# Performance work log

Hardware: AMD Instinct MI355X
Metric: run time of the kernel (lower is better)

The kernel has to match this reference:

```python
import jax, jax.numpy as jnp
import numpy as np

B, T, N, D = 16, 12, 512, 128
H, DH = 4, 32            # heads, per-head dim (out_dim = H*DH = 128)
E = 4096                  # edges in the static road graph
NEG_SLOPE = 0.2
LN_EPS = 1e-5


def setup_inputs() -> dict:
    key = jax.random.key(0)
    ks = jax.random.split(key, 9)
    x = jax.random.normal(ks[0], (B, T, N, D), dtype=jnp.float32)
    edge_index = jax.random.randint(ks[1], (2, E), 0, N, dtype=jnp.int64)
    edge_weight = jax.random.uniform(ks[2], (E,), dtype=jnp.float32)
    # GAT parameters (dropout in eval mode -> identity)
    W = jax.random.normal(ks[3], (D, H * DH), dtype=jnp.float32) * (1.0 / np.sqrt(D))
    att_src = jax.random.normal(ks[4], (H, DH), dtype=jnp.float32) * 0.1
    att_dst = jax.random.normal(ks[5], (H, DH), dtype=jnp.float32) * 0.1
    bias = jnp.zeros((H * DH,), dtype=jnp.float32)
    ln_gamma = jnp.ones((H * DH,), dtype=jnp.float32)
    ln_beta = jnp.zeros((H * DH,), dtype=jnp.float32)
    return {"x": x, "edge_index": edge_index, "edge_weight": edge_weight,
            "W": W, "att_src": att_src, "att_dst": att_dst, "bias": bias,
            "ln_gamma": ln_gamma, "ln_beta": ln_beta}


def reference(x, edge_index, edge_weight, W, att_src, att_dst, bias, ln_gamma, ln_beta):
    b, t, n, din = x.shape
    bt = b * t
    h_heads, dh = att_src.shape
    src, dst = edge_index[0], edge_index[1]

    # project: [BT, N, H, DH]
    h = (x.reshape(bt, n, din) @ W).reshape(bt, n, h_heads, dh)

    # per-node attention scores, then gather to edges: [BT, E, H]
    s_src = jnp.einsum('bnhd,hd->bnh', h, att_src)
    s_dst = jnp.einsum('bnhd,hd->bnh', h, att_dst)
    e = jax.nn.leaky_relu(s_src[:, src] + s_dst[:, dst], NEG_SLOPE)
    e = e * edge_weight[None, :, None]  # edge_weight modulates attention logits

    # scatter-softmax over incoming edges per destination node
    m = jnp.full((bt, n, h_heads), -1e30, dtype=e.dtype).at[:, dst].max(e)
    ex = jnp.exp(e - m[:, dst])
    denom = jnp.zeros((bt, n, h_heads), dtype=e.dtype).at[:, dst].add(ex)
    alpha = ex / (denom[:, dst] + 1e-16)  # [BT, E, H]

    # weighted aggregation (scatter-add) of source features
    msg = alpha[..., None] * h[:, src]  # [BT, E, H, DH]
    agg = jnp.zeros((bt, n, h_heads, dh), dtype=h.dtype).at[:, dst].add(msg)

    out = agg.reshape(b, t, n, h_heads * dh) + bias

    # LayerNorm then ELU
    mu = out.mean(axis=-1, keepdims=True)
    var = out.var(axis=-1, keepdims=True)
    out = (out - mu) * jax.lax.rsqrt(var + LN_EPS) * ln_gamma + ln_beta
    return jnp.where(out > 0, out, jnp.expm1(out))
```

## Files before the change

### kernel.cpp

```cpp
#include <hip/hip_runtime.h>

#define BT    192
#define NNODE 512
#define DIM   128
#define NH    4
#define DH    32
#define NE    4096
#define NROWS (BT * NNODE)

typedef __attribute__((ext_vector_type(8))) short  short8b;
typedef __attribute__((ext_vector_type(4))) float  floatx4;
typedef __attribute__((ext_vector_type(8))) unsigned short ushort8;

__device__ inline unsigned short f2bf(float f) {
    unsigned int u = __float_as_uint(f);
    return (unsigned short)((u + 0x7FFFu + ((u >> 16) & 1u)) >> 16);
}
__device__ inline float bflo(unsigned int v) { return __uint_as_float(v << 16); }
__device__ inline float bfhi(unsigned int v) { return __uint_as_float(v & 0xFFFF0000u); }

__device__ inline short8b pack8(float4 a, float4 b) {
    short8b r;
    r[0] = (short)f2bf(a.x); r[1] = (short)f2bf(a.y);
    r[2] = (short)f2bf(a.z); r[3] = (short)f2bf(a.w);
    r[4] = (short)f2bf(b.x); r[5] = (short)f2bf(b.y);
    r[6] = (short)f2bf(b.z); r[7] = (short)f2bf(b.w);
    return r;
}

__global__ __launch_bounds__(512) void csr_build_k(
    const int* __restrict__ ei, const float* __restrict__ ew,
    const float* __restrict__ W,
    int* __restrict__ row_ptr2, int* __restrict__ csr_src,
    float* __restrict__ csr_ew, int* __restrict__ perm,
    unsigned short* __restrict__ wswz)
{
    __shared__ int dsts[NE];
    __shared__ int cnt[NNODE];
    __shared__ int scan[NNODE];
    __shared__ int nodeAt[NNODE];
    __shared__ int hist[256];
    __shared__ int hscan[256];
    int t = threadIdx.x;
    int b = blockIdx.x;

    if (b >= 64) {
        int j = (b - 64) * 512 + t;
        const float4* W4 = (const float4*)W;
        float4 wv = W4[j];
        int k = j >> 5, c4 = (j & 31) * 4;
        float vv[4] = { wv.x, wv.y, wv.z, wv.w };
#pragma unroll
        for (int e = 0; e < 4; ++e) {
            int col = c4 + e;
            int byte = col * 256 + ((2 * k) ^ ((col & 7) << 4));
            wswz[byte >> 1] = f2bf(vv[e]);
        }
        return;
    }

    for (int e = t; e < NE; e += 512) dsts[e] = ei[NE + e];
    cnt[t] = 0;
    if (t < 256) hist[t] = 0;
    __syncthreads();
    for (int e = t; e < NE; e += 512) atomicAdd(&cnt[dsts[e]], 1);
    __syncthreads();

    int deg = cnt[t];
    int bkt = (deg < 255) ? deg : 255;
    atomicAdd(&hist[bkt], 1);
    __syncthreads();
    if (t < 256) hscan[t] = hist[t];
    __syncthreads();
    for (int o = 1; o < 256; o <<= 1) {
        int v = (t < 256 && t >= o) ? hscan[t - o] : 0;
        __syncthreads();
        if (t < 256) hscan[t] += v;
        __syncthreads();
    }
    int off = 0;
    for (int n = 0; n < t; ++n) {
        int dn = cnt[n]; dn = (dn < 255) ? dn : 255;
        off += (dn == bkt) ? 1 : 0;
    }
    int rank = hscan[bkt] - hist[bkt] + off;
    nodeAt[rank] = t;
    __syncthreads();

    scan[t] = cnt[nodeAt[t]];
    __syncthreads();
    for (int o = 1; o < NNODE; o <<= 1) {
        int v = (t >= o) ? scan[t - o] : 0;
        __syncthreads();
        scan[t] += v;
        __syncthreads();
    }
    if (b == 0) {
        if (t == 0) row_ptr2[0] = 0;
        row_ptr2[t + 1] = scan[t];
        perm[t] = nodeAt[t];
    }
    __syncthreads();

    int wave = t >> 6, lane = t & 63;
    int r = b * 8 + wave;
    int node = nodeAt[r];
    int pos = scan[r] - cnt[node];
    for (int c = 0; c < NE; c += 64) {
        int e = c + lane;
        int d = dsts[e];
        unsigned long long mask = __ballot(d == node);
        if (d == node) {
            int ofs = __popcll(mask & ((1ull << lane) - 1ull));
            csr_src[pos + ofs] = ei[e];
            csr_ew[pos + ofs]  = ew[e];
        }
        pos += __popcll(mask);
    }
}

__global__ __launch_bounds__(256) void gemm_mfma_k(
    const float* __restrict__ x, const unsigned short* __restrict__ wswz,
    const float* __restrict__ att_src, const float* __restrict__ att_dst,
    unsigned short* __restrict__ h, float* __restrict__ ssg,
    float* __restrict__ sdg)
{
    __shared__ __align__(16) char sm[64 * 132 * 4];
    __shared__ float att_f[256];
    int t = threadIdx.x;
    if (t < 128) att_f[t] = att_src[(t & 3) * 32 + (t >> 2)];
    else         att_f[t] = att_dst[(t & 3) * 32 + ((t - 128) >> 2)];
    {
        const uint4* g = (const uint4*)wswz;
        uint4* ld = (uint4*)sm;
#pragma unroll
        for (int i = 0; i < 8; ++i) ld[t + i * 256] = g[t + i * 256];
    }
    int w = t >> 6, l = t & 63, lr = l & 15, lk = l >> 4;
    size_t base = (size_t)blockIdx.x * 128;
    const float* xA = x + (base + (size_t)w * 16 + lr) * DIM;
    const float* xB = xA + 64 * DIM;

    floatx4 accA[8], accB[8];
#pragma unroll
    for (int n = 0; n < 8; ++n) {
        accA[n] = (floatx4){0.f, 0.f, 0.f, 0.f};
        accB[n] = (floatx4){0.f, 0.f, 0.f, 0.f};
    }
    __syncthreads();

#pragma unroll
    for (int kk = 0; kk < 4; ++kk) {
        int k0 = kk * 32 + lk * 8;
        float4 a0 = *(const float4*)(xA + k0);
        float4 a1 = *(const float4*)(xA + k0 + 4);
        float4 b0 = *(const float4*)(xB + k0);
        float4 b1 = *(const float4*)(xB + k0 + 4);
        short8b av = pack8(a0, a1);
        short8b bv = pack8(b0, b1);
        int c = kk * 4 + lk;
#pragma unroll
        for (int n = 0; n < 8; ++n) {
            int col = n * 16 + lr;
            short8b bf = *(const short8b*)(sm + col * 256 + ((c ^ (col & 7)) << 4));
            accA[n] = __builtin_amdgcn_mfma_f32_16x16x32_bf16(av, bf, accA[n], 0, 0, 0);
            accB[n] = __builtin_amdgcn_mfma_f32_16x16x32_bf16(bv, bf, accB[n], 0, 0, 0);
        }
    }

    float* Ct = (float*)sm;
    unsigned short* hbase = h + base * DIM;
    int sr = t >> 2, sq = t & 3;

    __syncthreads();
#pragma unroll
    for (int n = 0; n < 8; ++n)
#pragma unroll
        for (int j = 0; j < 4; ++j)
            Ct[(w * 16 + lk * 4 + j) * 132 + n * 16 + lr] = accA[n][j];
    __syncthreads();
#pragma unroll
    for (int i = 0; i < 4; ++i) {
        int chunk = t + i * 256;
        int row = chunk >> 4, cc = chunk & 15;
        const float* cp = Ct + row * 132 + cc * 8;
        ushort8 v;
#pragma unroll
        for (int e = 0; e < 8; ++e) v[e] = f2bf(cp[e]);
        *(ushort8*)(hbase + row * DIM + cc * 8) = v;
    }
    {
        const float* cp = Ct + sr * 132 + sq * 32;
        float ps = 0.f, pd = 0.f;
#pragma unroll
        for (int j = 0; j < 32; j += 4) {
            float4 cv = *(const float4*)(cp + j);
            ps = fmaf(cv.x, att_f[(j+0)*4 + sq], ps);
            ps = fmaf(cv.y, att_f[(j+1)*4 + sq], ps);
            ps = fmaf(cv.z, att_f[(j+2)*4 + sq], ps);
            ps = fmaf(cv.w, att_f[(j+3)*4 + sq], ps);
            pd = fmaf(cv.x, att_f[128 + (j+0)*4 + sq], pd);
            pd = fmaf(cv.y, att_f[128 + (j+1)*4 + sq], pd);
            pd = fmaf(cv.z, att_f[128 + (j+2)*4 + sq], pd);
            pd = fmaf(cv.w, att_f[128 + (j+3)*4 + sq], pd);
        }
        size_t grow = base + sr;
        ssg[grow * 4 + sq] = ps;
        sdg[grow * 4 + sq] = pd;
    }

    __syncthreads();
#pragma unroll
    for (int n = 0; n < 8; ++n)
#pragma unroll
        for (int j = 0; j < 4; ++j)
            Ct[(w * 16 + lk * 4 + j) * 132 + n * 16 + lr] = accB[n][j];
    __syncthreads();
#pragma unroll
    for (int i = 0; i < 4; ++i) {
        int chunk = t + i * 256;
        int row = chunk >> 4, cc = chunk & 15;
        const float* cp = Ct + row * 132 + cc * 8;
        ushort8 v;
#pragma unroll
        for (int e = 0; e < 8; ++e) v[e] = f2bf(cp[e]);
        *(ushort8*)(hbase + (64 + row) * DIM + cc * 8) = v;
    }
    {
        const float* cp = Ct + sr * 132 + sq * 32;
        float ps = 0.f, pd = 0.f;
#pragma unroll
        for (int j = 0; j < 32; j += 4) {
            float4 cv = *(const float4*)(cp + j);
            ps = fmaf(cv.x, att_f[(j+0)*4 + sq], ps);
            ps = fmaf(cv.y, att_f[(j+1)*4 + sq], ps);
            ps = fmaf(cv.z, att_f[(j+2)*4 + sq], ps);
            ps = fmaf(cv.w, att_f[(j+3)*4 + sq], ps);
            pd = fmaf(cv.x, att_f[128 + (j+0)*4 + sq], pd);
            pd = fmaf(cv.y, att_f[128 + (j+1)*4 + sq], pd);
            pd = fmaf(cv.z, att_f[128 + (j+2)*4 + sq], pd);
            pd = fmaf(cv.w, att_f[128 + (j+3)*4 + sq], pd);
        }
        size_t grow = base + 64 + sr;
        ssg[grow * 4 + sq] = ps;
        sdg[grow * 4 + sq] = pd;
    }
}

__global__ __launch_bounds__(1024) void agg_ln_k(
    const unsigned short* __restrict__ h,
    const float* __restrict__ ssg, const float* __restrict__ sdg,
    const int* __restrict__ rp2, const int* __restrict__ cs2,
    const float* __restrict__ ce2, const int* __restrict__ perm,
    const float* __restrict__ bias, const float* __restrict__ gamma,
    const float* __restrict__ beta, float* __restrict__ out)
{
    __shared__ unsigned int hs[NH][NNODE * 16];
    __shared__ float ssl[NNODE * NH];
    __shared__ float prm[384];
    int t  = threadIdx.x;
    int bt = blockIdx.x;

    const uint4* hg = (const uint4*)(h + (size_t)bt * NNODE * DIM);
    for (int i = t; i < NNODE * 16; i += 1024) {
        int n = i >> 4, c = i & 15, hh = c >> 2, j = c & 3;
        uint4 v = hg[i];
        int js = j ^ ((n >> 1) & 3);
        *(uint4*)&hs[hh][n * 16 + js * 4] = v;
    }
    const float* ssgb = ssg + (size_t)bt * NNODE * NH;
    for (int i = t; i < NNODE * NH; i += 1024) ssl[i] = ssgb[i];
    if (t < 384) prm[t] = (t < 128) ? bias[t] : (t < 256) ? gamma[t - 128] : beta[t - 256];
    __syncthreads();

    int l  = t & 63, w = t >> 6;
    int hh = l >> 4, rl = l & 15;
    int g  = w * 16 + rl;
    const float* sdgb = sdg + (size_t)bt * NNODE * NH;
    float* outb = out + (size_t)bt * NNODE * DIM;

#pragma unroll
    for (int pi = 0; pi < 2; ++pi) {
        int rank = pi ? (511 - g) : g;
        int node = perm[rank];
        int beg = rp2[rank], end = rp2[rank + 1];
        float sd = sdgb[node * 4 + hh];

        float acc[32];
#pragma unroll
        for (int d = 0; d < 32; ++d) acc[d] = 0.f;
        float den = 0.f;

        for (int e = beg; e < end; ++e) {
            int   s  = cs2[e];
            float wt = ce2[e];
            float a = ssl[s * 4 + hh] + sd;
            a = (a > 0.f) ? a : 0.2f * a;
            float p = __expf(a * wt);
            den += p;
            const unsigned int* hr = &hs[hh][s * 16];
            int sx = (s >> 1) & 3;
#pragma unroll
            for (int j = 0; j < 4; ++j) {
                uint4 v = *(const uint4*)&hr[(j ^ sx) * 4];
                int d0 = j * 8;
                acc[d0+0] = fmaf(p, bflo(v.x), acc[d0+0]);
                acc[d0+1] = fmaf(p, bfhi(v.x), acc[d0+1]);
                acc[d0+2] = fmaf(p, bflo(v.y), acc[d0+2]);
                acc[d0+3] = fmaf(p, bfhi(v.y), acc[d0+3]);
                acc[d0+4] = fmaf(p, bflo(v.z), acc[d0+4]);
                acc[d0+5] = fmaf(p, bfhi(v.z), acc[d0+5]);
                acc[d0+6] = fmaf(p, bflo(v.w), acc[d0+6]);
                acc[d0+7] = fmaf(p, bfhi(v.w), acc[d0+7]);
            }
        }

        float inv = 1.f / (den + 1e-16f);
        float s1 = 0.f, s2 = 0.f;
#pragma unroll
        for (int d = 0; d < 32; ++d) {
            float vv = fmaf(acc[d], inv, prm[hh * 32 + d]);
            acc[d] = vv;
            s1 += vv;
            s2 = fmaf(vv, vv, s2);
        }
        s1 += __shfl_xor(s1, 16, 64);
        s2 += __shfl_xor(s2, 16, 64);
        s1 += __shfl_xor(s1, 32, 64);
        s2 += __shfl_xor(s2, 32, 64);
        float mean = s1 * (1.f / 128.f);
        float var  = s2 * (1.f / 128.f) - mean * mean;
        float rstd = rsqrtf(var + 1e-5f);

        float* op = outb + (size_t)node * DIM + hh * 32;
#pragma unroll
        for (int d = 0; d < 32; d += 4) {
            int pd0 = 128 + hh * 32 + d, pb0 = 256 + hh * 32 + d;
            float y0 = (acc[d+0] - mean) * rstd * prm[pd0+0] + prm[pb0+0];
            float y1 = (acc[d+1] - mean) * rstd * prm[pd0+1] + prm[pb0+1];
            float y2 = (acc[d+2] - mean) * rstd * prm[pd0+2] + prm[pb0+2];
            float y3 = (acc[d+3] - mean) * rstd * prm[pd0+3] + prm[pb0+3];
            float4 o4;
            o4.x = (y0 > 0.f) ? y0 : expm1f(y0);
            o4.y = (y1 > 0.f) ? y1 : expm1f(y1);
            o4.z = (y2 > 0.f) ? y2 : expm1f(y2);
            o4.w = (y3 > 0.f) ? y3 : expm1f(y3);
            *(float4*)(op + d) = o4;
        }
    }
}

extern "C" void kernel_launch(void* const* d_in, const int* in_sizes, int n_in,
                              void* d_out, int out_size, void* d_ws, size_t ws_size,
                              hipStream_t stream)
{
    const float* x     = (const float*)d_in[0];
    const int*   ei    = (const int*)  d_in[1];
    const float* ew    = (const float*)d_in[2];
    const float* W     = (const float*)d_in[3];
    const float* asrc  = (const float*)d_in[4];
    const float* adst  = (const float*)d_in[5];
    const float* bias  = (const float*)d_in[6];
    const float* gamma = (const float*)d_in[7];
    const float* beta  = (const float*)d_in[8];
    float* out = (float*)d_out;

    char* ws = (char*)d_ws;
    unsigned short* h = (unsigned short*)ws;
    size_t off = (size_t)NROWS * DIM * sizeof(unsigned short);
    unsigned short* wswz = (unsigned short*)(ws + off);
    off += (size_t)DIM * DIM * sizeof(unsigned short);
    float* ssg = (float*)(ws + off);
    off += (size_t)NROWS * NH * sizeof(float);
    float* sdg = (float*)(ws + off);
    off += (size_t)NROWS * NH * sizeof(float);
    int* rp2 = (int*)(ws + off);
    off += (((NNODE + 1) * sizeof(int)) + 15) & ~(size_t)15;
    int* perm = (int*)(ws + off);
    off += (size_t)NNODE * sizeof(int);
    int* cs2 = (int*)(ws + off);
    off += (size_t)NE * sizeof(int);
    float* ce2 = (float*)(ws + off);
    off += (size_t)NE * sizeof(float);

    csr_build_k<<<72, 512, 0, stream>>>(ei, ew, W, rp2, cs2, ce2, perm, wswz);
    gemm_mfma_k<<<NROWS / 128, 256, 0, stream>>>(x, wswz, asrc, adst, h, ssg, sdg);
    agg_ln_k<<<BT, 1024, 0, stream>>>(h, ssg, sdg, rp2, cs2, ce2, perm,
                                      bias, gamma, beta, out);
}
```

Before: 73.24 us.

## Stage LayerNorm output through shared memory for coalesced row stores

The shared h buffer becomes one flat array laid out in two head-pair halves with an 8-way XOR swizzle, and it is reused after aggregation as a staging area for the output. Each thread keeps both passes' results in registers (64 floats), writes them to shared memory, then the block reads them back so that whole 512-byte node rows go out as contiguous float4 stores. The goal is better-coalesced global writes in place of per-thread 128-byte strided stores. In exchange the kernel needs more registers, extra barriers and extra shared-memory traffic.

```diff
diff --git a/kernel.cpp b/kernel.cpp
--- a/kernel.cpp
+++ b/kernel.cpp
@@ -255,18 +255,19 @@
     const float* __restrict__ bias, const float* __restrict__ gamma,
     const float* __restrict__ beta, float* __restrict__ out)
 {
-    __shared__ unsigned int hs[NH][NNODE * 16];
+    __shared__ __align__(16) unsigned int smem[NNODE * 64];
     __shared__ float ssl[NNODE * NH];
     __shared__ float prm[384];
     int t  = threadIdx.x;
     int bt = blockIdx.x;
 
     const uint4* hg = (const uint4*)(h + (size_t)bt * NNODE * DIM);
+    uint4* hs4 = (uint4*)smem;
     for (int i = t; i < NNODE * 16; i += 1024) {
-        int n = i >> 4, c = i & 15, hh = c >> 2, j = c & 3;
+        int n = i >> 4, c = i & 15;
         uint4 v = hg[i];
-        int js = j ^ ((n >> 1) & 3);
-        *(uint4*)&hs[hh][n * 16 + js * 4] = v;
+        int cp = (c & 7) ^ (n & 7);
+        hs4[(c >> 3) * 4096 + n * 8 + cp] = v;
     }
     const float* ssgb = ssg + (size_t)bt * NNODE * NH;
     for (int i = t; i < NNODE * NH; i += 1024) ssl[i] = ssgb[i];
@@ -276,8 +277,11 @@
     int l  = t & 63, w = t >> 6;
     int hh = l >> 4, rl = l & 15;
     int g  = w * 16 + rl;
+    int pair = hh >> 1, sub = hh & 1;
     const float* sdgb = sdg + (size_t)bt * NNODE * NH;
     float* outb = out + (size_t)bt * NNODE * DIM;
+
+    float y[2][32];
 
 #pragma unroll
     for (int pi = 0; pi < 2; ++pi) {
@@ -285,11 +289,9 @@
         int node = perm[rank];
         int beg = rp2[rank], end = rp2[rank + 1];
         float sd = sdgb[node * 4 + hh];
-
-        float acc[32];
-#pragma unroll
-        for (int d = 0; d < 32; ++d) acc[d] = 0.f;
         float den = 0.f;
+#pragma unroll
+        for (int d = 0; d < 32; ++d) y[pi][d] = 0.f;
 
         for (int e = beg; e < end; ++e) {
             int   s  = cs2[e];
@@ -298,20 +300,20 @@
             a = (a > 0.f) ? a : 0.2f * a;
             float p = __expf(a * wt);
             den += p;
-            const unsigned int* hr = &hs[hh][s * 16];
-            int sx = (s >> 1) & 3;
+            const uint4* hr = hs4 + pair * 4096 + s * 8;
+            int sx = s & 7;
 #pragma unroll
             for (int j = 0; j < 4; ++j) {
-                uint4 v = *(const uint4*)&hr[(j ^ sx) * 4];
+                uint4 v = hr[(sub * 4 + j) ^ sx];
                 int d0 = j * 8;
-                acc[d0+0] = fmaf(p, bflo(v.x), acc[d0+0]);
-                acc[d0+1] = fmaf(p, bfhi(v.x), acc[d0+1]);
-                acc[d0+2] = fmaf(p, bflo(v.y), acc[d0+2]);
-                acc[d0+3] = fmaf(p, bfhi(v.y), acc[d0+3]);
-                acc[d0+4] = fmaf(p, bflo(v.z), acc[d0+4]);
-                acc[d0+5] = fmaf(p, bfhi(v.z), acc[d0+5]);
-                acc[d0+6] = fmaf(p, bflo(v.w), acc[d0+6]);
-                acc[d0+7] = fmaf(p, bfhi(v.w), acc[d0+7]);
+                y[pi][d0+0] = fmaf(p, bflo(v.x), y[pi][d0+0]);
+                y[pi][d0+1] = fmaf(p, bfhi(v.x), y[pi][d0+1]);
+                y[pi][d0+2] = fmaf(p, bflo(v.y), y[pi][d0+2]);
+                y[pi][d0+3] = fmaf(p, bfhi(v.y), y[pi][d0+3]);
+                y[pi][d0+4] = fmaf(p, bflo(v.z), y[pi][d0+4]);
+                y[pi][d0+5] = fmaf(p, bfhi(v.z), y[pi][d0+5]);
+                y[pi][d0+6] = fmaf(p, bflo(v.w), y[pi][d0+6]);
+                y[pi][d0+7] = fmaf(p, bfhi(v.w), y[pi][d0+7]);
             }
         }
 
@@ -319,8 +321,8 @@
         float s1 = 0.f, s2 = 0.f;
 #pragma unroll
         for (int d = 0; d < 32; ++d) {
-            float vv = fmaf(acc[d], inv, prm[hh * 32 + d]);
-            acc[d] = vv;
+            float vv = fmaf(y[pi][d], inv, prm[hh * 32 + d]);
+            y[pi][d] = vv;
             s1 += vv;
             s2 = fmaf(vv, vv, s2);
         }
@@ -331,21 +333,33 @@
         float mean = s1 * (1.f / 128.f);
         float var  = s2 * (1.f / 128.f) - mean * mean;
         float rstd = rsqrtf(var + 1e-5f);
-
-        float* op = outb + (size_t)node * DIM + hh * 32;
-#pragma unroll
-        for (int d = 0; d < 32; d += 4) {
-            int pd0 = 128 + hh * 32 + d, pb0 = 256 + hh * 32 + d;
-            float y0 = (acc[d+0] - mean) * rstd * prm[pd0+0] + prm[pb0+0];
-            float y1 = (acc[d+1] - mean) * rstd * prm[pd0+1] + prm[pb0+1];
-            float y2 = (acc[d+2] - mean) * rstd * prm[pd0+2] + prm[pb0+2];
-            float y3 = (acc[d+3] - mean) * rstd * prm[pd0+3] + prm[pb0+3];
-            float4 o4;
-            o4.x = (y0 > 0.f) ? y0 : expm1f(y0);
-            o4.y = (y1 > 0.f) ? y1 : expm1f(y1);
-            o4.z = (y2 > 0.f) ? y2 : expm1f(y2);
-            o4.w = (y3 > 0.f) ? y3 : expm1f(y3);
-            *(float4*)(op + d) = o4;
+#pragma unroll
+        for (int d = 0; d < 32; ++d) {
+            float yy = (y[pi][d] - mean) * rstd * prm[128 + hh * 32 + d]
+                     + prm[256 + hh * 32 + d];
+            y[pi][d] = (yy > 0.f) ? yy : expm1f(yy);
+        }
+    }
+
+    float4* st = (float4*)smem;
+#pragma unroll
+    for (int pi = 0; pi < 2; ++pi) {
+        __syncthreads();
+#pragma unroll
+        for (int j = 0; j < 8; ++j) {
+            int m  = hh * 8 + j;
+            int mp = m ^ (g & 31);
+            float4 v = { y[pi][j*4+0], y[pi][j*4+1], y[pi][j*4+2], y[pi][j*4+3] };
+            st[g * 32 + mp] = v;
+        }
+        __syncthreads();
+#pragma unroll
+        for (int k = 0; k < 8; ++k) {
+            int c = t + k * 1024;
+            int r = c >> 5, m = c & 31;
+            float4 v = st[r * 32 + (m ^ (r & 31))];
+            int rank = pi ? (511 - r) : r;
+            *(float4*)(outb + (size_t)perm[rank] * DIM + m * 4) = v;
         }
     }
 }
```

Measured after the change: 77.90 us. 1.06x slower.

## Gather source rows from global memory instead of staging in LDS; split nodes across two blocks

Applied to the files above, without the earlier changes.

The aggregation kernel no longer copies each timestep's full h tile (128 KB of bf16) and source scores into shared memory. It gathers source rows directly from global memory, relying on cache. Work is split across twice as many blocks, each handling alternating degree ranks. The 4 heads of a node now sit in adjacent lanes, so the LayerNorm reduction uses shuffles at distances 1 and 2, and the edge loop is unrolled by two so more loads are in flight. This removes the LDS staging cost and the large LDS footprint that limited occupancy, at the cost of uncoalesced global gathers.

```diff
diff --git a/kernel.cpp b/kernel.cpp
--- a/kernel.cpp
+++ b/kernel.cpp
@@ -255,98 +255,113 @@
     const float* __restrict__ bias, const float* __restrict__ gamma,
     const float* __restrict__ beta, float* __restrict__ out)
 {
-    __shared__ unsigned int hs[NH][NNODE * 16];
-    __shared__ float ssl[NNODE * NH];
     __shared__ float prm[384];
-    int t  = threadIdx.x;
-    int bt = blockIdx.x;
-
-    const uint4* hg = (const uint4*)(h + (size_t)bt * NNODE * DIM);
-    for (int i = t; i < NNODE * 16; i += 1024) {
-        int n = i >> 4, c = i & 15, hh = c >> 2, j = c & 3;
-        uint4 v = hg[i];
-        int js = j ^ ((n >> 1) & 3);
-        *(uint4*)&hs[hh][n * 16 + js * 4] = v;
-    }
-    const float* ssgb = ssg + (size_t)bt * NNODE * NH;
-    for (int i = t; i < NNODE * NH; i += 1024) ssl[i] = ssgb[i];
+    int t = threadIdx.x;
     if (t < 384) prm[t] = (t < 128) ? bias[t] : (t < 256) ? gamma[t - 128] : beta[t - 256];
     __syncthreads();
 
-    int l  = t & 63, w = t >> 6;
-    int hh = l >> 4, rl = l & 15;
-    int g  = w * 16 + rl;
-    const float* sdgb = sdg + (size_t)bt * NNODE * NH;
-    float* outb = out + (size_t)bt * NNODE * DIM;
-
-#pragma unroll
-    for (int pi = 0; pi < 2; ++pi) {
-        int rank = pi ? (511 - g) : g;
-        int node = perm[rank];
-        int beg = rp2[rank], end = rp2[rank + 1];
-        float sd = sdgb[node * 4 + hh];
-
-        float acc[32];
-#pragma unroll
-        for (int d = 0; d < 32; ++d) acc[d] = 0.f;
-        float den = 0.f;
-
-        for (int e = beg; e < end; ++e) {
-            int   s  = cs2[e];
-            float wt = ce2[e];
-            float a = ssl[s * 4 + hh] + sd;
-            a = (a > 0.f) ? a : 0.2f * a;
-            float p = __expf(a * wt);
-            den += p;
-            const unsigned int* hr = &hs[hh][s * 16];
-            int sx = (s >> 1) & 3;
-#pragma unroll
-            for (int j = 0; j < 4; ++j) {
-                uint4 v = *(const uint4*)&hr[(j ^ sx) * 4];
-                int d0 = j * 8;
-                acc[d0+0] = fmaf(p, bflo(v.x), acc[d0+0]);
-                acc[d0+1] = fmaf(p, bfhi(v.x), acc[d0+1]);
-                acc[d0+2] = fmaf(p, bflo(v.y), acc[d0+2]);
-                acc[d0+3] = fmaf(p, bfhi(v.y), acc[d0+3]);
-                acc[d0+4] = fmaf(p, bflo(v.z), acc[d0+4]);
-                acc[d0+5] = fmaf(p, bfhi(v.z), acc[d0+5]);
-                acc[d0+6] = fmaf(p, bflo(v.w), acc[d0+6]);
-                acc[d0+7] = fmaf(p, bfhi(v.w), acc[d0+7]);
-            }
-        }
-
-        float inv = 1.f / (den + 1e-16f);
-        float s1 = 0.f, s2 = 0.f;
-#pragma unroll
-        for (int d = 0; d < 32; ++d) {
-            float vv = fmaf(acc[d], inv, prm[hh * 32 + d]);
-            acc[d] = vv;
-            s1 += vv;
-            s2 = fmaf(vv, vv, s2);
-        }
-        s1 += __shfl_xor(s1, 16, 64);
-        s2 += __shfl_xor(s2, 16, 64);
-        s1 += __shfl_xor(s1, 32, 64);
-        s2 += __shfl_xor(s2, 32, 64);
-        float mean = s1 * (1.f / 128.f);
-        float var  = s2 * (1.f / 128.f) - mean * mean;
-        float rstd = rsqrtf(var + 1e-5f);
-
-        float* op = outb + (size_t)node * DIM + hh * 32;
-#pragma unroll
-        for (int d = 0; d < 32; d += 4) {
-            int pd0 = 128 + hh * 32 + d, pb0 = 256 + hh * 32 + d;
-            float y0 = (acc[d+0] - mean) * rstd * prm[pd0+0] + prm[pb0+0];
-            float y1 = (acc[d+1] - mean) * rstd * prm[pd0+1] + prm[pb0+1];
-            float y2 = (acc[d+2] - mean) * rstd * prm[pd0+2] + prm[pb0+2];
-            float y3 = (acc[d+3] - mean) * rstd * prm[pd0+3] + prm[pb0+3];
-            float4 o4;
-            o4.x = (y0 > 0.f) ? y0 : expm1f(y0);
-            o4.y = (y1 > 0.f) ? y1 : expm1f(y1);
-            o4.z = (y2 > 0.f) ? y2 : expm1f(y2);
-            o4.w = (y3 > 0.f) ? y3 : expm1f(y3);
-            *(float4*)(op + d) = o4;
-        }
+    int bt   = blockIdx.x >> 1;
+    int par  = blockIdx.x & 1;
+    int hh   = t & 3;
+    int rank = ((t >> 2) << 1) + par;
+    int node = perm[rank];
+    int beg  = rp2[rank], end = rp2[rank + 1];
+
+    const unsigned short* hb = h + (size_t)bt * NNODE * DIM;
+    const float* ssb = ssg + (size_t)bt * NNODE * NH;
+    float sd = sdg[((size_t)bt * NNODE + node) * NH + hh];
+
+    float acc[32];
+#pragma unroll
+    for (int d = 0; d < 32; ++d) acc[d] = 0.f;
+    float den = 0.f;
+
+    int e = beg;
+    for (; e + 2 <= end; e += 2) {
+        int   s0 = cs2[e],   s1 = cs2[e + 1];
+        float w0 = ce2[e],   w1 = ce2[e + 1];
+        float a0 = ssb[s0 * 4 + hh] + sd; a0 = (a0 > 0.f) ? a0 : 0.2f * a0;
+        float a1 = ssb[s1 * 4 + hh] + sd; a1 = (a1 > 0.f) ? a1 : 0.2f * a1;
+        float p0 = __expf(a0 * w0);
+        float p1 = __expf(a1 * w1);
+        den += p0; den += p1;
+        const uint4* r0 = (const uint4*)(hb + (size_t)s0 * DIM) + hh * 4;
+        const uint4* r1 = (const uint4*)(hb + (size_t)s1 * DIM) + hh * 4;
+#pragma unroll
+        for (int j = 0; j < 4; ++j) {
+            uint4 v0 = r0[j];
+            uint4 v1 = r1[j];
+            int d0 = j * 8;
+            acc[d0+0] = fmaf(p0, bflo(v0.x), acc[d0+0]);
+            acc[d0+1] = fmaf(p0, bfhi(v0.x), acc[d0+1]);
+            acc[d0+2] = fmaf(p0, bflo(v0.y), acc[d0+2]);
+            acc[d0+3] = fmaf(p0, bfhi(v0.y), acc[d0+3]);
+            acc[d0+4] = fmaf(p0, bflo(v0.z), acc[d0+4]);
+            acc[d0+5] = fmaf(p0, bfhi(v0.z), acc[d0+5]);
+            acc[d0+6] = fmaf(p0, bflo(v0.w), acc[d0+6]);
+            acc[d0+7] = fmaf(p0, bfhi(v0.w), acc[d0+7]);
+            acc[d0+0] = fmaf(p1, bflo(v1.x), acc[d0+0]);
+            acc[d0+1] = fmaf(p1, bfhi(v1.x), acc[d0+1]);
+            acc[d0+2] = fmaf(p1, bflo(v1.y), acc[d0+2]);
+            acc[d0+3] = fmaf(p1, bfhi(v1.y), acc[d0+3]);
+            acc[d0+4] = fmaf(p1, bflo(v1.z), acc[d0+4]);
+            acc[d0+5] = fmaf(p1, bfhi(v1.z), acc[d0+5]);
+            acc[d0+6] = fmaf(p1, bflo(v1.w), acc[d0+6]);
+            acc[d0+7] = fmaf(p1, bfhi(v1.w), acc[d0+7]);
+        }
+    }
+    if (e < end) {
+        int   s0 = cs2[e];
+        float w0 = ce2[e];
+        float a0 = ssb[s0 * 4 + hh] + sd; a0 = (a0 > 0.f) ? a0 : 0.2f * a0;
+        float p0 = __expf(a0 * w0);
+        den += p0;
+        const uint4* r0 = (const uint4*)(hb + (size_t)s0 * DIM) + hh * 4;
+#pragma unroll
+        for (int j = 0; j < 4; ++j) {
+            uint4 v0 = r0[j];
+            int d0 = j * 8;
+            acc[d0+0] = fmaf(p0, bflo(v0.x), acc[d0+0]);
+            acc[d0+1] = fmaf(p0, bfhi(v0.x), acc[d0+1]);
+            acc[d0+2] = fmaf(p0, bflo(v0.y), acc[d0+2]);
+            acc[d0+3] = fmaf(p0, bfhi(v0.y), acc[d0+3]);
+            acc[d0+4] = fmaf(p0, bflo(v0.z), acc[d0+4]);
+            acc[d0+5] = fmaf(p0, bfhi(v0.z), acc[d0+5]);
+            acc[d0+6] = fmaf(p0, bflo(v0.w), acc[d0+6]);
+            acc[d0+7] = fmaf(p0, bfhi(v0.w), acc[d0+7]);
+        }
+    }
+
+    float inv = 1.f / (den + 1e-16f);
+    float s1 = 0.f, s2 = 0.f;
+#pragma unroll
+    for (int d = 0; d < 32; ++d) {
+        float vv = fmaf(acc[d], inv, prm[hh * 32 + d]);
+        acc[d] = vv;
+        s1 += vv;
+        s2 = fmaf(vv, vv, s2);
+    }
+    s1 += __shfl_xor(s1, 1, 64);
+    s2 += __shfl_xor(s2, 1, 64);
+    s1 += __shfl_xor(s1, 2, 64);
+    s2 += __shfl_xor(s2, 2, 64);
+    float mean = s1 * (1.f / 128.f);
+    float var  = s2 * (1.f / 128.f) - mean * mean;
+    float rstd = rsqrtf(var + 1e-5f);
+
+    float* op = out + ((size_t)bt * NNODE + node) * DIM + hh * 32;
+#pragma unroll
+    for (int d = 0; d < 32; d += 4) {
+        float y0 = (acc[d+0] - mean) * rstd * prm[128 + hh*32 + d+0] + prm[256 + hh*32 + d+0];
+        float y1 = (acc[d+1] - mean) * rstd * prm[128 + hh*32 + d+1] + prm[256 + hh*32 + d+1];
+        float y2 = (acc[d+2] - mean) * rstd * prm[128 + hh*32 + d+2] + prm[256 + hh*32 + d+2];
+        float y3 = (acc[d+3] - mean) * rstd * prm[128 + hh*32 + d+3] + prm[256 + hh*32 + d+3];
+        float4 o4;
+        o4.x = (y0 > 0.f) ? y0 : expm1f(y0);
+        o4.y = (y1 > 0.f) ? y1 : expm1f(y1);
+        o4.z = (y2 > 0.f) ? y2 : expm1f(y2);
+        o4.w = (y3 > 0.f) ? y3 : expm1f(y3);
+        *(float4*)(op + d) = o4;
     }
 }
 
@@ -385,6 +400,6 @@
 
     csr_build_k<<<72, 512, 0, stream>>>(ei, ew, W, rp2, cs2, ce2, perm, wswz);
     gemm_mfma_k<<<NROWS / 128, 256, 0, stream>>>(x, wswz, asrc, adst, h, ssg, sdg);
-    agg_ln_k<<<BT, 1024, 0, stream>>>(h, ssg, sdg, rp2, cs2, ce2, perm,
-                                      bias, gamma, beta, out);
-}
+    agg_ln_k<<<BT * 2, 1024, 0, stream>>>(h, ssg, sdg, rp2, cs2, ce2, perm,
+                                          bias, gamma, beta, out);
+}
```

Result: slower. 100.2 us (+36.8%).

## Fold CSR build into GEMM launch as extra blocks and unroll edge loop

Applied to the files above, without the earlier changes.

The CSR construction moves out of its own kernel and into 64 extra blocks of the GEMM launch. These blocks reuse the GEMM's shared memory and use 256 threads, each handling two nodes. A small kernel now only swizzles W to bf16, so the serial CSR build runs alongside the projection GEMM instead of before it. The aggregation edge loop is also unrolled by 4 so index loads and exps from several edges can overlap. In exchange the CSR blocks do twice the per-thread serial rank work, and the unrolled loop raises register pressure.

```diff
diff --git a/kernel.cpp b/kernel.cpp
--- a/kernel.cpp
+++ b/kernel.cpp
@@ -7,6 +7,7 @@
 #define DH    32
 #define NE    4096
 #define NROWS (BT * NNODE)
+#define GEMM_BLOCKS (NROWS / 128)
 
 typedef __attribute__((ext_vector_type(8))) short  short8b;
 typedef __attribute__((ext_vector_type(4))) float  floatx4;
@@ -28,94 +29,34 @@
     return r;
 }
 
-__global__ __launch_bounds__(512) void csr_build_k(
-    const int* __restrict__ ei, const float* __restrict__ ew,
-    const float* __restrict__ W,
-    int* __restrict__ row_ptr2, int* __restrict__ csr_src,
-    float* __restrict__ csr_ew, int* __restrict__ perm,
-    unsigned short* __restrict__ wswz)
+#define EDGE_ACC(hrow, sx, p) do {                                   \
+    _Pragma("unroll")                                                \
+    for (int j = 0; j < 4; ++j) {                                    \
+        uint4 v = *(const uint4*)&(hrow)[(j ^ (sx)) * 4];            \
+        int d0 = j * 8;                                              \
+        acc[d0+0] = fmaf((p), bflo(v.x), acc[d0+0]);                 \
+        acc[d0+1] = fmaf((p), bfhi(v.x), acc[d0+1]);                 \
+        acc[d0+2] = fmaf((p), bflo(v.y), acc[d0+2]);                 \
+        acc[d0+3] = fmaf((p), bfhi(v.y), acc[d0+3]);                 \
+        acc[d0+4] = fmaf((p), bflo(v.z), acc[d0+4]);                 \
+        acc[d0+5] = fmaf((p), bfhi(v.z), acc[d0+5]);                 \
+        acc[d0+6] = fmaf((p), bflo(v.w), acc[d0+6]);                 \
+        acc[d0+7] = fmaf((p), bfhi(v.w), acc[d0+7]);                 \
+    } } while (0)
+
+__global__ __launch_bounds__(512) void wswz_k(
+    const float* __restrict__ W, unsigned short* __restrict__ wswz)
 {
-    __shared__ int dsts[NE];
-    __shared__ int cnt[NNODE];
-    __shared__ int scan[NNODE];
-    __shared__ int nodeAt[NNODE];
-    __shared__ int hist[256];
-    __shared__ int hscan[256];
-    int t = threadIdx.x;
-    int b = blockIdx.x;
-
-    if (b >= 64) {
-        int j = (b - 64) * 512 + t;
-        const float4* W4 = (const float4*)W;
-        float4 wv = W4[j];
-        int k = j >> 5, c4 = (j & 31) * 4;
-        float vv[4] = { wv.x, wv.y, wv.z, wv.w };
-#pragma unroll
-        for (int e = 0; e < 4; ++e) {
-            int col = c4 + e;
-            int byte = col * 256 + ((2 * k) ^ ((col & 7) << 4));
-            wswz[byte >> 1] = f2bf(vv[e]);
-        }
-        return;
-    }
-
-    for (int e = t; e < NE; e += 512) dsts[e] = ei[NE + e];
-    cnt[t] = 0;
-    if (t < 256) hist[t] = 0;
-    __syncthreads();
-    for (int e = t; e < NE; e += 512) atomicAdd(&cnt[dsts[e]], 1);
-    __syncthreads();
-
-    int deg = cnt[t];
-    int bkt = (deg < 255) ? deg : 255;
-    atomicAdd(&hist[bkt], 1);
-    __syncthreads();
-    if (t < 256) hscan[t] = hist[t];
-    __syncthreads();
-    for (int o = 1; o < 256; o <<= 1) {
-        int v = (t < 256 && t >= o) ? hscan[t - o] : 0;
-        __syncthreads();
-        if (t < 256) hscan[t] += v;
-        __syncthreads();
-    }
-    int off = 0;
-    for (int n = 0; n < t; ++n) {
-        int dn = cnt[n]; dn = (dn < 255) ? dn : 255;
-        off += (dn == bkt) ? 1 : 0;
-    }
-    int rank = hscan[bkt] - hist[bkt] + off;
-    nodeAt[rank] = t;
-    __syncthreads();
-
-    scan[t] = cnt[nodeAt[t]];
-    __syncthreads();
-    for (int o = 1; o < NNODE; o <<= 1) {
-        int v = (t >= o) ? scan[t - o] : 0;
-        __syncthreads();
-        scan[t] += v;
-        __syncthreads();
-    }
-    if (b == 0) {
-        if (t == 0) row_ptr2[0] = 0;
-        row_ptr2[t + 1] = scan[t];
-        perm[t] = nodeAt[t];
-    }
-    __syncthreads();
-
-    int wave = t >> 6, lane = t & 63;
-    int r = b * 8 + wave;
-    int node = nodeAt[r];
-    int pos = scan[r] - cnt[node];
-    for (int c = 0; c < NE; c += 64) {
-        int e = c + lane;
-        int d = dsts[e];
-        unsigned long long mask = __ballot(d == node);
-        if (d == node) {
-            int ofs = __popcll(mask & ((1ull << lane) - 1ull));
-            csr_src[pos + ofs] = ei[e];
-            csr_ew[pos + ofs]  = ew[e];
-        }
-        pos += __popcll(mask);
+    int j = blockIdx.x * 512 + threadIdx.x;
+    const float4* W4 = (const float4*)W;
+    float4 wv = W4[j];
+    int k = j >> 5, c4 = (j & 31) * 4;
+    float vv[4] = { wv.x, wv.y, wv.z, wv.w };
+#pragma unroll
+    for (int e = 0; e < 4; ++e) {
+        int col = c4 + e;
+        int byte = col * 256 + ((2 * k) ^ ((col & 7) << 4));
+        wswz[byte >> 1] = f2bf(vv[e]);
     }
 }
 
@@ -123,11 +64,101 @@
     const float* __restrict__ x, const unsigned short* __restrict__ wswz,
     const float* __restrict__ att_src, const float* __restrict__ att_dst,
     unsigned short* __restrict__ h, float* __restrict__ ssg,
-    float* __restrict__ sdg)
+    float* __restrict__ sdg,
+    const int* __restrict__ ei, const float* __restrict__ ew,
+    int* __restrict__ rp2, int* __restrict__ cs2,
+    float* __restrict__ ce2, int* __restrict__ perm)
 {
     __shared__ __align__(16) char sm[64 * 132 * 4];
     __shared__ float att_f[256];
     int t = threadIdx.x;
+
+    if (blockIdx.x >= GEMM_BLOCKS) {
+        int* dsts   = (int*)sm;
+        int* cnt    = (int*)(sm + 16384);
+        int* scn    = (int*)(sm + 18432);
+        int* nodeAt = (int*)(sm + 20480);
+        int* hist   = (int*)(sm + 22528);
+        int* hscan  = (int*)(sm + 23552);
+        int cb = blockIdx.x - GEMM_BLOCKS;
+        int i0 = t, i1 = t + 256;
+
+        for (int e = t; e < NE; e += 256) dsts[e] = ei[NE + e];
+        cnt[i0] = 0; cnt[i1] = 0;
+        hist[t] = 0;
+        __syncthreads();
+        for (int e = t; e < NE; e += 256) atomicAdd(&cnt[dsts[e]], 1);
+        __syncthreads();
+
+        int deg0 = cnt[i0], deg1 = cnt[i1];
+        int b0 = (deg0 < 255) ? deg0 : 255;
+        int b1 = (deg1 < 255) ? deg1 : 255;
+        atomicAdd(&hist[b0], 1);
+        atomicAdd(&hist[b1], 1);
+        __syncthreads();
+        hscan[t] = hist[t];
+        __syncthreads();
+        for (int o = 1; o < 256; o <<= 1) {
+            int v = (t >= o) ? hscan[t - o] : 0;
+            __syncthreads();
+            hscan[t] += v;
+            __syncthreads();
+        }
+        int off0 = 0, off1 = 0;
+        for (int n = 0; n < i0; ++n) {
+            int dn = cnt[n]; dn = (dn < 255) ? dn : 255;
+            off0 += (dn == b0) ? 1 : 0;
+        }
+        for (int n = 0; n < i1; ++n) {
+            int dn = cnt[n]; dn = (dn < 255) ? dn : 255;
+            off1 += (dn == b1) ? 1 : 0;
+        }
+        int rank0 = hscan[b0] - hist[b0] + off0;
+        int rank1 = hscan[b1] - hist[b1] + off1;
+        nodeAt[rank0] = i0;
+        nodeAt[rank1] = i1;
+        __syncthreads();
+
+        scn[i0] = cnt[nodeAt[i0]];
+        scn[i1] = cnt[nodeAt[i1]];
+        __syncthreads();
+        for (int o = 1; o < NNODE; o <<= 1) {
+            int v0 = (i0 >= o) ? scn[i0 - o] : 0;
+            int v1 = (i1 >= o) ? scn[i1 - o] : 0;
+            __syncthreads();
+            scn[i0] += v0; scn[i1] += v1;
+            __syncthreads();
+        }
+        if (cb == 0) {
+            if (t == 0) rp2[0] = 0;
+            rp2[i0 + 1] = scn[i0];
+            rp2[i1 + 1] = scn[i1];
+            perm[i0] = nodeAt[i0];
+            perm[i1] = nodeAt[i1];
+        }
+        __syncthreads();
+
+        int wave = t >> 6, lane = t & 63;
+#pragma unroll
+        for (int rr = 0; rr < 2; ++rr) {
+            int r = cb * 8 + rr * 4 + wave;
+            int node = nodeAt[r];
+            int pos = scn[r] - cnt[node];
+            for (int c = 0; c < NE; c += 64) {
+                int e = c + lane;
+                int d = dsts[e];
+                unsigned long long mask = __ballot(d == node);
+                if (d == node) {
+                    int ofs = __popcll(mask & ((1ull << lane) - 1ull));
+                    cs2[pos + ofs] = ei[e];
+                    ce2[pos + ofs] = ew[e];
+                }
+                pos += __popcll(mask);
+            }
+        }
+        return;
+    }
+
     if (t < 128) att_f[t] = att_src[(t & 3) * 32 + (t >> 2)];
     else         att_f[t] = att_dst[(t & 3) * 32 + ((t - 128) >> 2)];
     {
@@ -291,28 +322,41 @@
         for (int d = 0; d < 32; ++d) acc[d] = 0.f;
         float den = 0.f;
 
-        for (int e = beg; e < end; ++e) {
-            int   s  = cs2[e];
-            float wt = ce2[e];
-            float a = ssl[s * 4 + hh] + sd;
-            a = (a > 0.f) ? a : 0.2f * a;
-            float p = __expf(a * wt);
-            den += p;
-            const unsigned int* hr = &hs[hh][s * 16];
-            int sx = (s >> 1) & 3;
-#pragma unroll
-            for (int j = 0; j < 4; ++j) {
-                uint4 v = *(const uint4*)&hr[(j ^ sx) * 4];
-                int d0 = j * 8;
-                acc[d0+0] = fmaf(p, bflo(v.x), acc[d0+0]);
-                acc[d0+1] = fmaf(p, bfhi(v.x), acc[d0+1]);
-                acc[d0+2] = fmaf(p, bflo(v.y), acc[d0+2]);
-                acc[d0+3] = fmaf(p, bfhi(v.y), acc[d0+3]);
-                acc[d0+4] = fmaf(p, bflo(v.z), acc[d0+4]);
-                acc[d0+5] = fmaf(p, bfhi(v.z), acc[d0+5]);
-                acc[d0+6] = fmaf(p, bflo(v.w), acc[d0+6]);
-                acc[d0+7] = fmaf(p, bfhi(v.w), acc[d0+7]);
-            }
+        int e = beg;
+        for (; e + 4 <= end; e += 4) {
+            int   s0 = cs2[e],     s1 = cs2[e + 1];
+            int   s2 = cs2[e + 2], s3 = cs2[e + 3];
+            float w0 = ce2[e],     w1 = ce2[e + 1];
+            float w2 = ce2[e + 2], w3 = ce2[e + 3];
+            float a0 = ssl[s0 * 4 + hh] + sd; a0 = (a0 > 0.f) ? a0 : 0.2f * a0;
+            float a1 = ssl[s1 * 4 + hh] + sd; a1 = (a1 > 0.f) ? a1 : 0.2f * a1;
+            float a2 = ssl[s2 * 4 + hh] + sd; a2 = (a2 > 0.f) ? a2 : 0.2f * a2;
+            float a3 = ssl[s3 * 4 + hh] + sd; a3 = (a3 > 0.f) ? a3 : 0.2f * a3;
+            float p0 = __expf(a0 * w0);
+            float p1 = __expf(a1 * w1);
+            float p2 = __expf(a2 * w2);
+            float p3 = __expf(a3 * w3);
+            den += p0; den += p1; den += p2; den += p3;
+            const unsigned int* r0 = &hs[hh][s0 * 16];
+            const unsigned int* r1 = &hs[hh][s1 * 16];
+            const unsigned int* r2 = &hs[hh][s2 * 16];
+            const unsigned int* r3 = &hs[hh][s3 * 16];
+            int x0 = (s0 >> 1) & 3, x1 = (s1 >> 1) & 3;
+            int x2 = (s2 >> 1) & 3, x3 = (s3 >> 1) & 3;
+            EDGE_ACC(r0, x0, p0);
+            EDGE_ACC(r1, x1, p1);
+            EDGE_ACC(r2, x2, p2);
+            EDGE_ACC(r3, x3, p3);
+        }
+        for (; e < end; ++e) {
+            int   s0 = cs2[e];
+            float w0 = ce2[e];
+            float a0 = ssl[s0 * 4 + hh] + sd; a0 = (a0 > 0.f) ? a0 : 0.2f * a0;
+            float p0 = __expf(a0 * w0);
+            den += p0;
+            const unsigned int* r0 = &hs[hh][s0 * 16];
+            int x0 = (s0 >> 1) & 3;
+            EDGE_ACC(r0, x0, p0);
         }
 
         float inv = 1.f / (den + 1e-16f);
@@ -383,8 +427,9 @@
     float* ce2 = (float*)(ws + off);
     off += (size_t)NE * sizeof(float);
 
-    csr_build_k<<<72, 512, 0, stream>>>(ei, ew, W, rp2, cs2, ce2, perm, wswz);
-    gemm_mfma_k<<<NROWS / 128, 256, 0, stream>>>(x, wswz, asrc, adst, h, ssg, sdg);
+    wswz_k<<<8, 512, 0, stream>>>(W, wswz);
+    gemm_mfma_k<<<GEMM_BLOCKS + 64, 256, 0, stream>>>(
+        x, wswz, asrc, adst, h, ssg, sdg, ei, ew, rp2, cs2, ce2, perm);
     agg_ln_k<<<BT, 1024, 0, stream>>>(h, ssg, sdg, rp2, cs2, ce2, perm,
                                       bias, gamma, beta, out);
 }
```

Result: slower. 99.88 us (+36.4%).
